# Performance work log

Measured on AMD Instinct MI355X. Metric: run time of the kernel, lower is better.

Reference implementation:

```python
import jax, jax.numpy as jnp
import numpy as np

N_NODES = 100000
N_EDGES = 3200000
IN_CH = 128
HID = 64
N_GRAPHS = 512


def _gcn_conv(x, W, b, src, dst, n_nodes):
    """PyG GCNConv: out = D^{-1/2} (A + I) D^{-1/2} X W + b.
    src/dst are edge endpoints; self-loops handled analytically."""
    h = x @ W  # [N, out]
    # degree with self-loops (count at target nodes, as in PyG)
    deg = jnp.zeros((n_nodes,), h.dtype).at[dst].add(1.0) + 1.0
    dis = jax.lax.rsqrt(deg)  # deg^{-1/2}
    norm = dis[src] * dis[dst]  # [E]
    msg = h[src] * norm[:, None]  # gather + scale, [E, out]
    out = jnp.zeros_like(h).at[dst].add(msg)  # scatter-add
    # self-loop term: norm_ii = 1/deg_i
    out = out + h * (dis * dis)[:, None]
    return out + b


def setup_inputs() -> dict:
    key = jax.random.key(0)
    ks = jax.random.split(key, 8)
    x = jax.random.normal(ks[0], (N_NODES, IN_CH), dtype=jnp.float32)
    edge_index = jax.random.randint(ks[1], (2, N_EDGES), 0, N_NODES, dtype=jnp.int64)
    batch = jnp.sort(jax.random.randint(ks[2], (N_NODES,), 0, N_GRAPHS, dtype=jnp.int64))
    s1 = 1.0 / np.sqrt(IN_CH)
    s2 = 1.0 / np.sqrt(HID)
    W1 = jax.random.uniform(ks[3], (IN_CH, HID), jnp.float32, -s1, s1)
    b1 = jax.random.uniform(ks[4], (HID,), jnp.float32, -s1, s1)
    W2 = jax.random.uniform(ks[5], (HID, HID), jnp.float32, -s2, s2)
    b2 = jax.random.uniform(ks[6], (HID,), jnp.float32, -s2, s2)
    return {"x": x, "edge_index": edge_index, "batch": batch,
            "W1": W1, "b1": b1, "W2": W2, "b2": b2}


def reference(x, edge_index, batch, W1, b1, W2, b2):
    src, dst = edge_index[0], edge_index[1]
    n = x.shape[0]
    h = jax.nn.relu(_gcn_conv(x, W1, b1, src, dst, n))
    h = jax.nn.relu(_gcn_conv(h, W2, b2, src, dst, n))
    # F.dropout(p=0.2) treated as identity (eval / deterministic reference)
    # global_mean_pool: segment mean over graph ids
    sums = jax.ops.segment_sum(h, batch, num_segments=N_GRAPHS)
    cnts = jax.ops.segment_sum(jnp.ones((n,), h.dtype), batch, num_segments=N_GRAPHS)
    return sums / jnp.maximum(cnts, 1.0)[:, None]
```

## Files before the change

### kernel.cpp

```cpp
#include <hip/hip_runtime.h>

typedef unsigned int uint;

#define N_NODES 100000
#define N_EDGES 3200000
#define IN_CH 128
#define HID 64
#define N_GRAPHS 512
#define EPB 4096
#define NBLK ((N_EDGES + EPB - 1) / EPB)
#define NB 391
#define CAP 10240

__device__ __forceinline__ uint f2bf1(float f) {
    union { float f; uint i; } v; v.f = f;
    return (v.i + 0x7fffu + ((v.i >> 16) & 1u)) >> 16;
}
__device__ __forceinline__ uint pack2(float lo, float hi) {
    return f2bf1(lo) | (f2bf1(hi) << 16);
}
__device__ __forceinline__ float2 ub2(uint u) {
    union { uint i; float f; } a, b;
    a.i = u << 16; b.i = u & 0xffff0000u;
    return make_float2(a.f, b.f);
}
__device__ __forceinline__ void bacc(uint u, float& lo, float& hi) {
    float2 f = ub2(u);
    lo += f.x; hi += f.y;
}

__global__ __launch_bounds__(256) void scatter_kernel(const int* __restrict__ src,
                                                      const int* __restrict__ dst,
                                                      int* __restrict__ bcnt,
                                                      uint* __restrict__ pairs) {
    __shared__ int h[4 * NB];
    __shared__ int start[NB];
    __shared__ int cur[NB];
    int t = threadIdx.x;
    int base = blockIdx.x * EPB;

    int rs[16], rd[16];
#pragma unroll
    for (int j = 0; j < 16; ++j) {
        int e = base + j * 256 + t;
        if (e < N_EDGES) { rs[j] = src[e]; rd[j] = dst[e]; }
        else rd[j] = -1;
    }
    for (int i = t; i < 4 * NB; i += 256) h[i] = 0;
    __syncthreads();
    int w = t >> 6;
#pragma unroll
    for (int j = 0; j < 16; ++j)
        if (rd[j] >= 0) atomicAdd(&h[w * NB + (rd[j] >> 8)], 1);
    __syncthreads();
    for (int b = t; b < NB; b += 256) {
        int tot = h[b] + h[NB + b] + h[2 * NB + b] + h[3 * NB + b];
        start[b] = tot ? atomicAdd(&bcnt[b * 16], tot) : 0;
        cur[b] = 0;
    }
    __syncthreads();
#pragma unroll
    for (int j = 0; j < 16; ++j) {
        if (rd[j] >= 0) {
            int b = rd[j] >> 8;
            int r = atomicAdd(&cur[b], 1);
            pairs[(size_t)b * CAP + start[b] + r] =
                ((uint)(rd[j] & 255) << 24) | (uint)rs[j];
        }
    }
}

__global__ __launch_bounds__(256) void bucket_csr_kernel(const uint* __restrict__ pairs,
                                                         const int* __restrict__ bcnt,
                                                         int* __restrict__ csr_src,
                                                         int* __restrict__ rstart,
                                                         int* __restrict__ rend,
                                                         float* __restrict__ dis) {
    __shared__ int h[256];
    int b = blockIdx.x;
    int t = threadIdx.x;
    int e0 = b * CAP;
    int e1 = e0 + bcnt[b * 16];
    h[t] = 0;
    __syncthreads();
    for (int e = e0 + t; e < e1; e += 256)
        atomicAdd(&h[pairs[e] >> 24], 1);
    __syncthreads();
    int v = h[t];
#pragma unroll
    for (int o = 1; o < 256; o <<= 1) {
        int x = (t >= o) ? h[t - o] : 0;
        __syncthreads();
        h[t] += x;
        __syncthreads();
    }
    int excl = h[t] - v;
    int n = b * 256 + t;
    if (n < N_NODES) {
        rstart[n] = e0 + excl;
        rend[n] = e0 + excl + v;
        dis[n] = rsqrtf((float)v + 1.0f);
    }
    __syncthreads();
    h[t] = e0 + excl;
    __syncthreads();
    for (int e = e0 + t; e < e1; e += 256) {
        uint p = pairs[e];
        int pos = atomicAdd(&h[p >> 24], 1);
        csr_src[pos] = (int)(p & 0xFFFFFFu);
    }
}

__global__ __launch_bounds__(256) void gemm1_kernel(const float* __restrict__ X,
                                                    const float* __restrict__ W,
                                                    const float* __restrict__ dis,
                                                    uint* __restrict__ Y) {
    __shared__ float Wl[IN_CH * 64];
    __shared__ float Xs[128 * 33];
    int t = threadIdx.x;
    for (int idx = t; idx < IN_CH * 64; idx += 256) Wl[idx] = W[idx];

    int r0 = (t >> 3) * 4;
    int c0 = (t & 7) * 8;
    int rowBase = blockIdx.x * 128;

    float acc[4][8];
#pragma unroll
    for (int a = 0; a < 4; ++a)
#pragma unroll
        for (int c = 0; c < 8; ++c) acc[a][c] = 0.f;

    int srow = t >> 1;
    int shh = (t & 1) * 16;
    bool sok = (rowBase + srow) < N_NODES;
    const float* xbase = X + (size_t)(rowBase + srow) * IN_CH + shh;

    float4 nx[4];
#pragma unroll
    for (int f = 0; f < 4; ++f)
        nx[f] = sok ? *reinterpret_cast<const float4*>(xbase + f * 4)
                    : make_float4(0.f, 0.f, 0.f, 0.f);

    for (int kc = 0; kc < IN_CH; kc += 32) {
        if (kc) __syncthreads();
#pragma unroll
        for (int f = 0; f < 4; ++f) {
            int o = srow * 33 + shh + f * 4;
            Xs[o] = nx[f].x; Xs[o + 1] = nx[f].y; Xs[o + 2] = nx[f].z; Xs[o + 3] = nx[f].w;
        }
        __syncthreads();
        if (kc + 32 < IN_CH) {
#pragma unroll
            for (int f = 0; f < 4; ++f)
                nx[f] = sok ? *reinterpret_cast<const float4*>(xbase + kc + 32 + f * 4)
                            : make_float4(0.f, 0.f, 0.f, 0.f);
        }
#pragma unroll
        for (int kk = 0; kk < 32; ++kk) {
            const float4 wa = *reinterpret_cast<const float4*>(&Wl[(kc + kk) * 64 + c0]);
            const float4 wb = *reinterpret_cast<const float4*>(&Wl[(kc + kk) * 64 + c0 + 4]);
            float xr[4];
#pragma unroll
            for (int a = 0; a < 4; ++a) xr[a] = Xs[(r0 + a) * 33 + kk];
#pragma unroll
            for (int a = 0; a < 4; ++a) {
                acc[a][0] += xr[a] * wa.x; acc[a][1] += xr[a] * wa.y;
                acc[a][2] += xr[a] * wa.z; acc[a][3] += xr[a] * wa.w;
                acc[a][4] += xr[a] * wb.x; acc[a][5] += xr[a] * wb.y;
                acc[a][6] += xr[a] * wb.z; acc[a][7] += xr[a] * wb.w;
            }
        }
    }
#pragma unroll
    for (int a = 0; a < 4; ++a) {
        int row = rowBase + r0 + a;
        if (row < N_NODES) {
            float d = dis[row];
            uint4 o;
            o.x = pack2(acc[a][0] * d, acc[a][1] * d);
            o.y = pack2(acc[a][2] * d, acc[a][3] * d);
            o.z = pack2(acc[a][4] * d, acc[a][5] * d);
            o.w = pack2(acc[a][6] * d, acc[a][7] * d);
            *reinterpret_cast<uint4*>(Y + (size_t)row * 32 + (t & 7) * 4) = o;
        }
    }
}

__global__ __launch_bounds__(256) void gemm2_kernel(const uint* __restrict__ X,
                                                    const float* __restrict__ W,
                                                    const float* __restrict__ dis,
                                                    uint* __restrict__ Y) {
    __shared__ float Wl[HID * 64];
    __shared__ float Xs[128 * 33];
    int t = threadIdx.x;
    for (int idx = t; idx < HID * 64; idx += 256) Wl[idx] = W[idx];

    int r0 = (t >> 3) * 4;
    int c0 = (t & 7) * 8;
    int rowBase = blockIdx.x * 128;

    float acc[4][8];
#pragma unroll
    for (int a = 0; a < 4; ++a)
#pragma unroll
        for (int c = 0; c < 8; ++c) acc[a][c] = 0.f;

    int srow = t >> 1;
    int shh = (t & 1) * 16;
    bool sok = (rowBase + srow) < N_NODES;
    const uint* xbase = X + (size_t)(rowBase + srow) * 32 + (t & 1) * 8;

    uint4 n0_ = make_uint4(0, 0, 0, 0), n1_ = n0_;
    if (sok) {
        n0_ = *reinterpret_cast<const uint4*>(xbase);
        n1_ = *reinterpret_cast<const uint4*>(xbase + 4);
    }

    for (int kc = 0; kc < HID; kc += 32) {
        if (kc) __syncthreads();
        {
            uint us[8] = {n0_.x, n0_.y, n0_.z, n0_.w, n1_.x, n1_.y, n1_.z, n1_.w};
            int o = srow * 33 + shh;
#pragma unroll
            for (int j = 0; j < 8; ++j) {
                float2 f = ub2(us[j]);
                Xs[o + 2 * j]     = fmaxf(f.x, 0.f);
                Xs[o + 2 * j + 1] = fmaxf(f.y, 0.f);
            }
        }
        __syncthreads();
        if (kc + 32 < HID && sok) {
            n0_ = *reinterpret_cast<const uint4*>(xbase + 16);
            n1_ = *reinterpret_cast<const uint4*>(xbase + 20);
        }
#pragma unroll
        for (int kk = 0; kk < 32; ++kk) {
            const float4 wa = *reinterpret_cast<const float4*>(&Wl[(kc + kk) * 64 + c0]);
            const float4 wb = *reinterpret_cast<const float4*>(&Wl[(kc + kk) * 64 + c0 + 4]);
            float xr[4];
#pragma unroll
            for (int a = 0; a < 4; ++a) xr[a] = Xs[(r0 + a) * 33 + kk];
#pragma unroll
            for (int a = 0; a < 4; ++a) {
                acc[a][0] += xr[a] * wa.x; acc[a][1] += xr[a] * wa.y;
                acc[a][2] += xr[a] * wa.z; acc[a][3] += xr[a] * wa.w;
                acc[a][4] += xr[a] * wb.x; acc[a][5] += xr[a] * wb.y;
                acc[a][6] += xr[a] * wb.z; acc[a][7] += xr[a] * wb.w;
            }
        }
    }
#pragma unroll
    for (int a = 0; a < 4; ++a) {
        int row = rowBase + r0 + a;
        if (row < N_NODES) {
            float d = dis[row];
            uint4 o;
            o.x = pack2(acc[a][0] * d, acc[a][1] * d);
            o.y = pack2(acc[a][2] * d, acc[a][3] * d);
            o.z = pack2(acc[a][4] * d, acc[a][5] * d);
            o.w = pack2(acc[a][6] * d, acc[a][7] * d);
            *reinterpret_cast<uint4*>(Y + (size_t)row * 32 + (t & 7) * 4) = o;
        }
    }
}

__global__ __launch_bounds__(256) void gather_kernel(const int* __restrict__ rstart,
                                                     const int* __restrict__ rend,
                                                     const int* __restrict__ csr_src,
                                                     const float* __restrict__ dis,
                                                     const float* __restrict__ bias,
                                                     const uint* __restrict__ A,
                                                     uint* __restrict__ B) {
    int i = blockIdx.x * 4 + (threadIdx.x >> 6);
    if (i >= N_NODES) return;
    int lane = threadIdx.x & 63;
    int q = lane >> 3;
    int cu = (lane & 7) * 4;

    float4 bi0 = *reinterpret_cast<const float4*>(&bias[(lane & 7) * 8]);
    float4 bi1 = *reinterpret_cast<const float4*>(&bias[(lane & 7) * 8 + 4]);

    int e = rstart[i];
    int end = rend[i];

    float a[8], b[8];
#pragma unroll
    for (int j = 0; j < 8; ++j) { a[j] = 0.f; b[j] = 0.f; }

    if (q == 0) {
        uint4 u = *reinterpret_cast<const uint4*>(&A[(size_t)i * 32 + cu]);
        bacc(u.x, a[0], a[1]); bacc(u.y, a[2], a[3]);
        bacc(u.z, a[4], a[5]); bacc(u.w, a[6], a[7]);
    }
    for (; e + 16 <= end; e += 16) {
        int s0 = csr_src[e + q];
        int s1 = csr_src[e + 8 + q];
        uint4 u0 = *reinterpret_cast<const uint4*>(&A[(size_t)s0 * 32 + cu]);
        uint4 u1 = *reinterpret_cast<const uint4*>(&A[(size_t)s1 * 32 + cu]);
        bacc(u0.x, a[0], a[1]); bacc(u0.y, a[2], a[3]);
        bacc(u0.z, a[4], a[5]); bacc(u0.w, a[6], a[7]);
        bacc(u1.x, b[0], b[1]); bacc(u1.y, b[2], b[3]);
        bacc(u1.z, b[4], b[5]); bacc(u1.w, b[6], b[7]);
    }
    for (; e + 8 <= end; e += 8) {
        int s = csr_src[e + q];
        uint4 u = *reinterpret_cast<const uint4*>(&A[(size_t)s * 32 + cu]);
        bacc(u.x, a[0], a[1]); bacc(u.y, a[2], a[3]);
        bacc(u.z, a[4], a[5]); bacc(u.w, a[6], a[7]);
    }
    if (e + q < end) {
        int s = csr_src[e + q];
        uint4 u = *reinterpret_cast<const uint4*>(&A[(size_t)s * 32 + cu]);
        bacc(u.x, b[0], b[1]); bacc(u.y, b[2], b[3]);
        bacc(u.z, b[4], b[5]); bacc(u.w, b[6], b[7]);
    }
#pragma unroll
    for (int j = 0; j < 8; ++j) {
        a[j] += b[j];
        a[j] += __shfl_xor(a[j], 8);
        a[j] += __shfl_xor(a[j], 16);
        a[j] += __shfl_xor(a[j], 32);
    }
    if (q == 0) {
        float d = dis[i];
        uint4 o;
        o.x = pack2(bi0.x + d * a[0], bi0.y + d * a[1]);
        o.y = pack2(bi0.z + d * a[2], bi0.w + d * a[3]);
        o.z = pack2(bi1.x + d * a[4], bi1.y + d * a[5]);
        o.w = pack2(bi1.z + d * a[6], bi1.w + d * a[7]);
        *reinterpret_cast<uint4*>(B + (size_t)i * 32 + (lane & 7) * 4) = o;
    }
}

__global__ __launch_bounds__(256) void pool_kernel(const uint* __restrict__ B,
                                                   const int* __restrict__ batch,
                                                   float* __restrict__ sums,
                                                   float* __restrict__ cnt) {
    int w = blockIdx.x * 4 + (threadIdx.x >> 6);
    int half = (threadIdx.x >> 5) & 1;
    int l = threadIdx.x & 31;
    int n0 = w * 32 + half * 16;
    if (n0 >= N_NODES) return;
    int n1 = min(n0 + 16, N_NODES);
    int curg = batch[n0];
    float a0 = 0.f, a1 = 0.f;
    int run = 0;
    for (int n = n0; n < n1; ++n) {
        int g = batch[n];
        if (g != curg) {
            atomicAdd(&sums[curg * 64 + 2 * l], a0);
            atomicAdd(&sums[curg * 64 + 2 * l + 1], a1);
            if (l == 0) atomicAdd(&cnt[curg], (float)run);
            curg = g; a0 = 0.f; a1 = 0.f; run = 0;
        }
        float2 f = ub2(B[(size_t)n * 32 + l]);
        a0 += fmaxf(f.x, 0.f);
        a1 += fmaxf(f.y, 0.f);
        run++;
    }
    atomicAdd(&sums[curg * 64 + 2 * l], a0);
    atomicAdd(&sums[curg * 64 + 2 * l + 1], a1);
    if (l == 0) atomicAdd(&cnt[curg], (float)run);
}

__global__ __launch_bounds__(256) void final_kernel(const float* __restrict__ sums,
                                                    const float* __restrict__ cnt,
                                                    float* __restrict__ out) {
    int idx = blockIdx.x * 256 + threadIdx.x;
    if (idx < N_GRAPHS * 64) out[idx] = sums[idx] / fmaxf(cnt[idx >> 6], 1.0f);
}

extern "C" void kernel_launch(void* const* d_in, const int* in_sizes, int n_in,
                              void* d_out, int out_size, void* d_ws, size_t ws_size,
                              hipStream_t stream) {
    const float* x     = (const float*)d_in[0];
    const int*   edge  = (const int*)d_in[1];
    const int*   batch = (const int*)d_in[2];
    const float* W1    = (const float*)d_in[3];
    const float* b1    = (const float*)d_in[4];
    const float* W2    = (const float*)d_in[5];
    const float* b2    = (const float*)d_in[6];
    float* out = (float*)d_out;

    uint*  A        = (uint*)d_ws;
    uint*  B        = A + (size_t)N_NODES * 32;
    uint*  pairs    = B + (size_t)N_NODES * 32;
    int*   csr_src  = (int*)(pairs + (size_t)NB * CAP);
    float* dis      = (float*)(csr_src + (size_t)NB * CAP);
    int*   rstart   = (int*)(dis + N_NODES);
    int*   rend     = rstart + N_NODES;
    float* sums     = (float*)(rend + N_NODES);
    float* cnt_f    = sums + (size_t)N_GRAPHS * 64;
    int*   bcnt     = (int*)(cnt_f + N_GRAPHS);

    const int* src = edge;
    const int* dst = edge + N_EDGES;

    hipMemsetAsync(sums, 0, (N_GRAPHS * 64 + N_GRAPHS + NB * 16) * sizeof(float), stream);

    scatter_kernel<<<NBLK, 256, 0, stream>>>(src, dst, bcnt, pairs);
    bucket_csr_kernel<<<NB, 256, 0, stream>>>(pairs, bcnt, csr_src, rstart, rend, dis);

    gemm1_kernel<<<(N_NODES + 127) / 128, 256, 0, stream>>>(x, W1, dis, A);
    gather_kernel<<<(N_NODES + 3) / 4, 256, 0, stream>>>(rstart, rend, csr_src, dis, b1, A, B);

    gemm2_kernel<<<(N_NODES + 127) / 128, 256, 0, stream>>>(B, W2, dis, A);
    gather_kernel<<<(N_NODES + 3) / 4, 256, 0, stream>>>(rstart, rend, csr_src, dis, b2, A, B);

    pool_kernel<<<(N_NODES + 127) / 128, 256, 0, stream>>>(B, batch, sums, cnt_f);
    final_kernel<<<(N_GRAPHS * 64 + 255) / 256, 256, 0, stream>>>(sums, cnt_f, out);
}
```

Baseline: 366.2 us.

## Halve CSR bucket width to 128 nodes and pack aggregation adds

```diff
diff --git a/kernel.cpp b/kernel.cpp
--- a/kernel.cpp
+++ b/kernel.cpp
@@ -1,6 +1,7 @@
 #include <hip/hip_runtime.h>
 
 typedef unsigned int uint;
+typedef float f32x2 __attribute__((ext_vector_type(2)));
 
 #define N_NODES 100000
 #define N_EDGES 3200000
@@ -9,8 +10,8 @@
 #define N_GRAPHS 512
 #define EPB 4096
 #define NBLK ((N_EDGES + EPB - 1) / EPB)
-#define NB 391
-#define CAP 10240
+#define NB 782
+#define CAP 4608
 
 __device__ __forceinline__ uint f2bf1(float f) {
     union { float f; uint i; } v; v.f = f;
@@ -24,9 +25,11 @@
     a.i = u << 16; b.i = u & 0xffff0000u;
     return make_float2(a.f, b.f);
 }
-__device__ __forceinline__ void bacc(uint u, float& lo, float& hi) {
-    float2 f = ub2(u);
-    lo += f.x; hi += f.y;
+__device__ __forceinline__ f32x2 up2(uint u) {
+    union { uint i; float f; } lo, hi;
+    lo.i = u << 16; hi.i = u & 0xffff0000u;
+    f32x2 r; r.x = lo.f; r.y = hi.f;
+    return r;
 }
 
 __global__ __launch_bounds__(256) void scatter_kernel(const int* __restrict__ src,
@@ -51,7 +54,7 @@
     int w = t >> 6;
 #pragma unroll
     for (int j = 0; j < 16; ++j)
-        if (rd[j] >= 0) atomicAdd(&h[w * NB + (rd[j] >> 8)], 1);
+        if (rd[j] >= 0) atomicAdd(&h[w * NB + (rd[j] >> 7)], 1);
     __syncthreads();
     for (int b = t; b < NB; b += 256) {
         int tot = h[b] + h[NB + b] + h[2 * NB + b] + h[3 * NB + b];
@@ -62,10 +65,10 @@
 #pragma unroll
     for (int j = 0; j < 16; ++j) {
         if (rd[j] >= 0) {
-            int b = rd[j] >> 8;
+            int b = rd[j] >> 7;
             int r = atomicAdd(&cur[b], 1);
             pairs[(size_t)b * CAP + start[b] + r] =
-                ((uint)(rd[j] & 255) << 24) | (uint)rs[j];
+                ((uint)(rd[j] & 127) << 24) | (uint)rs[j];
         }
     }
 }
@@ -76,33 +79,33 @@
                                                          int* __restrict__ rstart,
                                                          int* __restrict__ rend,
                                                          float* __restrict__ dis) {
-    __shared__ int h[256];
+    __shared__ int h[128];
     int b = blockIdx.x;
     int t = threadIdx.x;
     int e0 = b * CAP;
     int e1 = e0 + bcnt[b * 16];
-    h[t] = 0;
+    if (t < 128) h[t] = 0;
     __syncthreads();
     for (int e = e0 + t; e < e1; e += 256)
         atomicAdd(&h[pairs[e] >> 24], 1);
     __syncthreads();
-    int v = h[t];
-#pragma unroll
-    for (int o = 1; o < 256; o <<= 1) {
-        int x = (t >= o) ? h[t - o] : 0;
+    int v = (t < 128) ? h[t] : 0;
+#pragma unroll
+    for (int o = 1; o < 128; o <<= 1) {
+        int x = (t >= o && t < 128) ? h[t - o] : 0;
         __syncthreads();
-        h[t] += x;
+        if (t < 128) h[t] += x;
         __syncthreads();
     }
-    int excl = h[t] - v;
-    int n = b * 256 + t;
-    if (n < N_NODES) {
+    int excl = (t < 128) ? h[t] - v : 0;
+    int n = b * 128 + t;
+    if (t < 128 && n < N_NODES) {
         rstart[n] = e0 + excl;
         rend[n] = e0 + excl + v;
         dis[n] = rsqrtf((float)v + 1.0f);
     }
     __syncthreads();
-    h[t] = e0 + excl;
+    if (t < 128) h[t] = e0 + excl;
     __syncthreads();
     for (int e = e0 + t; e < e1; e += 256) {
         uint p = pairs[e];
@@ -283,51 +286,51 @@
     int e = rstart[i];
     int end = rend[i];
 
-    float a[8], b[8];
-#pragma unroll
-    for (int j = 0; j < 8; ++j) { a[j] = 0.f; b[j] = 0.f; }
+    f32x2 a[4], b[4];
+#pragma unroll
+    for (int j = 0; j < 4; ++j) { a[j] = (f32x2)0.f; b[j] = (f32x2)0.f; }
 
     if (q == 0) {
         uint4 u = *reinterpret_cast<const uint4*>(&A[(size_t)i * 32 + cu]);
-        bacc(u.x, a[0], a[1]); bacc(u.y, a[2], a[3]);
-        bacc(u.z, a[4], a[5]); bacc(u.w, a[6], a[7]);
+        a[0] += up2(u.x); a[1] += up2(u.y); a[2] += up2(u.z); a[3] += up2(u.w);
     }
     for (; e + 16 <= end; e += 16) {
         int s0 = csr_src[e + q];
         int s1 = csr_src[e + 8 + q];
         uint4 u0 = *reinterpret_cast<const uint4*>(&A[(size_t)s0 * 32 + cu]);
         uint4 u1 = *reinterpret_cast<const uint4*>(&A[(size_t)s1 * 32 + cu]);
-        bacc(u0.x, a[0], a[1]); bacc(u0.y, a[2], a[3]);
-        bacc(u0.z, a[4], a[5]); bacc(u0.w, a[6], a[7]);
-        bacc(u1.x, b[0], b[1]); bacc(u1.y, b[2], b[3]);
-        bacc(u1.z, b[4], b[5]); bacc(u1.w, b[6], b[7]);
+        a[0] += up2(u0.x); a[1] += up2(u0.y); a[2] += up2(u0.z); a[3] += up2(u0.w);
+        b[0] += up2(u1.x); b[1] += up2(u1.y); b[2] += up2(u1.z); b[3] += up2(u1.w);
     }
     for (; e + 8 <= end; e += 8) {
         int s = csr_src[e + q];
         uint4 u = *reinterpret_cast<const uint4*>(&A[(size_t)s * 32 + cu]);
-        bacc(u.x, a[0], a[1]); bacc(u.y, a[2], a[3]);
-        bacc(u.z, a[4], a[5]); bacc(u.w, a[6], a[7]);
+        a[0] += up2(u.x); a[1] += up2(u.y); a[2] += up2(u.z); a[3] += up2(u.w);
     }
     if (e + q < end) {
         int s = csr_src[e + q];
         uint4 u = *reinterpret_cast<const uint4*>(&A[(size_t)s * 32 + cu]);
-        bacc(u.x, b[0], b[1]); bacc(u.y, b[2], b[3]);
-        bacc(u.z, b[4], b[5]); bacc(u.w, b[6], b[7]);
+        b[0] += up2(u.x); b[1] += up2(u.y); b[2] += up2(u.z); b[3] += up2(u.w);
+    }
+    float r[8];
+#pragma unroll
+    for (int j = 0; j < 4; ++j) {
+        f32x2 s = a[j] + b[j];
+        r[2 * j] = s.x; r[2 * j + 1] = s.y;
     }
 #pragma unroll
     for (int j = 0; j < 8; ++j) {
-        a[j] += b[j];
-        a[j] += __shfl_xor(a[j], 8);
-        a[j] += __shfl_xor(a[j], 16);
-        a[j] += __shfl_xor(a[j], 32);
+        r[j] += __shfl_xor(r[j], 8);
+        r[j] += __shfl_xor(r[j], 16);
+        r[j] += __shfl_xor(r[j], 32);
     }
     if (q == 0) {
         float d = dis[i];
         uint4 o;
-        o.x = pack2(bi0.x + d * a[0], bi0.y + d * a[1]);
-        o.y = pack2(bi0.z + d * a[2], bi0.w + d * a[3]);
-        o.z = pack2(bi1.x + d * a[4], bi1.y + d * a[5]);
-        o.w = pack2(bi1.z + d * a[6], bi1.w + d * a[7]);
+        o.x = pack2(bi0.x + d * r[0], bi0.y + d * r[1]);
+        o.y = pack2(bi0.z + d * r[2], bi0.w + d * r[3]);
+        o.z = pack2(bi1.x + d * r[4], bi1.y + d * r[5]);
+        o.w = pack2(bi1.z + d * r[6], bi1.w + d * r[7]);
         *reinterpret_cast<uint4*>(B + (size_t)i * 32 + (lane & 7) * 4) = o;
     }
 }
```

New measurement: 379.8 us. 3.7% more time.
